# Kernel tuning notes

Hardware: AMD Instinct MI355X
Metric: run time of the kernel (lower is better)

Reference implementation:

```python
import jax, jax.numpy as jnp
import numpy as np

N_QUBITS = 9
N_CIR = 8
CHUNK = 256  # 2**(N_QUBITS-1)
DIM = 512    # 2**N_QUBITS

# Fixed gate sequence (kind, param_index, wires) transcribed from the qnode.
GATES = []
GATES += [("ry", i, (i,)) for i in range(9)]
GATES += [("rx", 9 + i, (i,)) for i in range(9)]
GATES += [("xx", 18 + k, w) for k, w in enumerate([(0,1),(8,7),(1,2),(7,6),(2,3),(6,5),(3,4),(5,4)])]
GATES += [("cry", 26 + k, w) for k, w in enumerate([(0,1),(1,2),(2,3),(8,7),(7,6),(6,5),(5,4),(3,4)])]
GATES += [("ry", 34 + i, (i,)) for i in range(9)]
GATES += [("xy", 43 + k, w) for k, w in enumerate([(4,3),(4,5),(3,2),(5,6),(2,1),(6,7),(1,0),(7,8)])]
GATES += [("crx", 51 + k, w) for k, w in enumerate([(0,1),(2,3),(5,6),(7,8),(1,2),(6,7)])]
GATES += [("rx", 57 + i, (i,)) for i in range(9)]
GATES += [("xx", 66 + k, w) for k, w in enumerate([(0,1),(8,7),(1,2),(7,6),(2,3),(6,5),(3,4),(5,4)])]
GATES += [("cry", 74 + k, w) for k, w in enumerate([(0,1),(1,2),(2,3),(8,7),(7,6),(6,5),(5,4),(3,4)])]
GATES += [("ry", 82 + i, (i,)) for i in range(9)]
GATES += [("xy", 91 + k, w) for k, w in enumerate([(4,3),(4,5),(3,2),(5,6),(2,1),(6,7),(1,0),(7,8)])]
GATES += [("crx", 99 + k, w) for k, w in enumerate([(0,1),(2,3),(5,6),(7,8),(1,2),(6,7)])]
GATES += [("rx", 105 + i, (i,)) for i in range(9)]
assert len(GATES) == 114

C64 = jnp.complex64

def _ry(t):
    c = jnp.cos(t / 2).astype(C64); s = jnp.sin(t / 2).astype(C64)
    return jnp.stack([jnp.stack([c, -s]), jnp.stack([s, c])])

def _rx(t):
    c = jnp.cos(t / 2).astype(C64); s = (-1j * jnp.sin(t / 2)).astype(C64)
    return jnp.stack([jnp.stack([c, s]), jnp.stack([s, c])])

def _xx(t):  # exp(-i t/2 XX)
    c = jnp.cos(t / 2).astype(C64); s = (-1j * jnp.sin(t / 2)).astype(C64)
    z = jnp.zeros_like(c)
    return jnp.stack([jnp.stack([c, z, z, s]), jnp.stack([z, c, s, z]),
                      jnp.stack([z, s, c, z]), jnp.stack([s, z, z, c])])

def _xy(t):  # PennyLane IsingXY
    c = jnp.cos(t / 2).astype(C64); s = (1j * jnp.sin(t / 2)).astype(C64)
    o = jnp.ones_like(c); z = jnp.zeros_like(c)
    return jnp.stack([jnp.stack([o, z, z, z]), jnp.stack([z, c, s, z]),
                      jnp.stack([z, s, c, z]), jnp.stack([z, z, z, o])])

def _ctrl(u2):  # block-diag(I2, u2): control on wires[0], target wires[1]
    z2 = jnp.zeros((2, 2), u2.dtype); i2 = jnp.eye(2, dtype=u2.dtype)
    return jnp.concatenate([jnp.concatenate([i2, z2], 1), jnp.concatenate([z2, u2], 1)], 0)

def _apply1(st, u, w):
    ax = 1 + w
    t = jnp.moveaxis(st, ax, -1)
    t = jnp.einsum('...a,ba->...b', t, u)
    return jnp.moveaxis(t, -1, ax)

def _apply2(st, u, w0, w1):
    a0, a1 = 1 + w0, 1 + w1
    t = jnp.moveaxis(st, (a0, a1), (-2, -1))
    sh = t.shape
    t = jnp.einsum('...a,ba->...b', t.reshape(sh[:-2] + (4,)), u).reshape(sh)
    return jnp.moveaxis(t, (-2, -1), (a0, a1))

def _circuit_probs(feats, qw):
    # feats: (N, 256) float32 -> analytic probs (N, 512)
    f = feats / jnp.linalg.norm(feats, axis=-1, keepdims=True)
    N = f.shape[0]
    # AmplitudeEmbedding on wires [0,1,2,3,5,6,7,8]; wire 4 stays |0>.
    st = jnp.stack([f.reshape(N, 16, 16), jnp.zeros((N, 16, 16), f.dtype)], axis=2)
    st = st.reshape((N,) + (2,) * N_QUBITS).astype(C64)
    for kind, idx, w in GATES:
        t = qw[idx]
        if kind == 'ry':
            st = _apply1(st, _ry(t), w[0])
        elif kind == 'rx':
            st = _apply1(st, _rx(t), w[0])
        elif kind == 'xx':
            st = _apply2(st, _xx(t), *w)
        elif kind == 'xy':
            st = _apply2(st, _xy(t), *w)
        elif kind == 'cry':
            st = _apply2(st, _ctrl(_ry(t)), *w)
        else:  # crx
            st = _apply2(st, _ctrl(_rx(t)), *w)
    return (st.real ** 2 + st.imag ** 2).reshape(N, DIM).astype(jnp.float32)


def setup_inputs() -> dict:
    key = jax.random.key(0)
    k1, k2 = jax.random.split(key)
    B = 4096
    return {
        "input_features": jax.random.normal(k1, (B, N_CIR * CHUNK), dtype=jnp.float32),
        "q_params": jax.random.normal(k2, (114,), dtype=jnp.float32),  # q_delta=1
    }


def reference(input_features, q_params):
    B = input_features.shape[0]
    q_in = jnp.tanh(input_features) * (np.pi / 2.0)
    chunks = q_in.reshape(B * N_CIR, CHUNK)          # per-sample split into 8 chunks of 256
    probs = _circuit_probs(chunks, q_params)          # (B*8, 512), all circuits batched
    return probs.reshape(B, 1024, 2, 2)
```

## Files before the change

### kernel.cpp

```cpp
#include <hip/hip_runtime.h>
#include <utility>

typedef __attribute__((ext_vector_type(8))) short short8;
typedef __attribute__((ext_vector_type(4))) float f32x4;
typedef unsigned short u16;

#define NROW 32768
#define KDIM 256
#define NOUT 512

static constexpr unsigned char cGK[114] = {
  0,0,0,0,0,0,0,0,0,
  1,1,1,1,1,1,1,1,1,
  2,2,2,2,2,2,2,2,
  4,4,4,4,4,4,4,4,
  0,0,0,0,0,0,0,0,0,
  3,3,3,3,3,3,3,3,
  5,5,5,5,5,5,
  1,1,1,1,1,1,1,1,1,
  2,2,2,2,2,2,2,2,
  4,4,4,4,4,4,4,4,
  0,0,0,0,0,0,0,0,0,
  3,3,3,3,3,3,3,3,
  5,5,5,5,5,5,
  1,1,1,1,1,1,1,1,1
};
static constexpr unsigned char cGW0[114] = {
  0,1,2,3,4,5,6,7,8,
  0,1,2,3,4,5,6,7,8,
  0,8,1,7,2,6,3,5,
  0,1,2,8,7,6,5,3,
  0,1,2,3,4,5,6,7,8,
  4,4,3,5,2,6,1,7,
  0,2,5,7,1,6,
  0,1,2,3,4,5,6,7,8,
  0,8,1,7,2,6,3,5,
  0,1,2,8,7,6,5,3,
  0,1,2,3,4,5,6,7,8,
  4,4,3,5,2,6,1,7,
  0,2,5,7,1,6,
  0,1,2,3,4,5,6,7,8
};
static constexpr unsigned char cGW1[114] = {
  0,0,0,0,0,0,0,0,0,
  0,0,0,0,0,0,0,0,0,
  1,7,2,6,3,5,4,4,
  1,2,3,7,6,5,4,4,
  0,0,0,0,0,0,0,0,0,
  3,5,2,6,1,7,0,8,
  1,3,6,8,2,7,
  0,0,0,0,0,0,0,0,0,
  1,7,2,6,3,5,4,4,
  1,2,3,7,6,5,4,4,
  0,0,0,0,0,0,0,0,0,
  3,5,2,6,1,7,0,8,
  1,3,6,8,2,7,
  0,0,0,0,0,0,0,0,0
};

__device__ __forceinline__ u16 f2bf(float f) {
  unsigned int u = __float_as_uint(f);
  u = (u + 0x7fffu + ((u >> 16) & 1u)) >> 16;
  return (u16)u;
}
__device__ __forceinline__ float bf2f(u16 b) {
  return __uint_as_float(((unsigned int)b) << 16);
}

__device__ __forceinline__ float fast_tanh(float x) {
  float xc = fminf(x, 15.f);
  float e = __expf(2.f * xc);
  return 1.f - 2.f * __builtin_amdgcn_rcpf(e + 1.f);
}

typedef const __attribute__((address_space(1))) unsigned int* gptr_t;
typedef __attribute__((address_space(3))) unsigned int* lptr_t;
__device__ __forceinline__ void gload16(const void* g, void* l) {
  __builtin_amdgcn_global_load_lds((gptr_t)g, (lptr_t)l, 16, 0, 0);
}

template <int G>
__device__ __forceinline__ void apply_gate(float (&re)[8], float (&im)[8],
                                           float c0v, float s0v, float c1v,
                                           float s1v, int l) {
  constexpr int kind = cGK[G];
  constexpr int p0 = 8 - cGW0[G];
  constexpr int p1 = 8 - cGW1[G];
  constexpr int m = (kind <= 1) ? (1 << p0)
                  : (kind <= 3) ? ((1 << p0) | (1 << p1))
                  : (1 << p1);
  constexpr int ml = m & 63;
  constexpr int mr = m >> 6;
  float c = __shfl((G < 64) ? c0v : c1v, G & 63, 64);
  float s = __shfl((G < 64) ? s0v : s1v, G & 63, 64);
  float br[8], bi[8];
  #pragma unroll
  for (int r = 0; r < 8; ++r) { br[r] = re[r ^ mr]; bi[r] = im[r ^ mr]; }
  if constexpr (ml != 0) {
    #pragma unroll
    for (int r = 0; r < 8; ++r) {
      br[r] = __shfl_xor(br[r], ml, 64);
      bi[r] = __shfl_xor(bi[r], ml, 64);
    }
  }
  #pragma unroll
  for (int r = 0; r < 8; ++r) {
    const int idx = (r << 6) | l;
    float nre, nim;
    if constexpr (kind == 0) {
      float sg = ((idx >> p0) & 1) ? s : -s;
      nre = c * re[r] + sg * br[r];
      nim = c * im[r] + sg * bi[r];
    } else if constexpr (kind == 1 || kind == 2) {
      nre = c * re[r] + s * bi[r];
      nim = c * im[r] - s * br[r];
    } else if constexpr (kind == 3) {
      bool ap = (((idx >> p0) ^ (idx >> p1)) & 1) != 0;
      nre = ap ? (c * re[r] - s * bi[r]) : re[r];
      nim = ap ? (c * im[r] + s * br[r]) : im[r];
    } else if constexpr (kind == 4) {
      bool ap = ((idx >> p0) & 1) != 0;
      float sg = ((idx >> p1) & 1) ? s : -s;
      nre = ap ? (c * re[r] + sg * br[r]) : re[r];
      nim = ap ? (c * im[r] + sg * bi[r]) : im[r];
    } else {
      bool ap = ((idx >> p0) & 1) != 0;
      nre = ap ? (c * re[r] + s * bi[r]) : re[r];
      nim = ap ? (c * im[r] - s * br[r]) : im[r];
    }
    re[r] = nre; im[r] = nim;
  }
}

template <int... Gs>
__device__ __forceinline__ void apply_all(std::integer_sequence<int, Gs...>,
                                          float (&re)[8], float (&im)[8],
                                          float c0v, float s0v, float c1v,
                                          float s1v, int l) {
  (apply_gate<Gs>(re, im, c0v, s0v, c1v, s1v, l), ...);
}

__global__ void __launch_bounds__(256) build_b(const float* __restrict__ qp,
                                               u16* __restrict__ BreT,
                                               u16* __restrict__ BimT) {
  int tid = threadIdx.x;
  int l = tid & 63;
  int k = blockIdx.x * 4 + (tid >> 6);
  float a0 = qp[l] * 0.5f;
  float a1 = (l < 50) ? qp[l + 64] * 0.5f : 0.f;
  float c0v = cosf(a0), s0v = sinf(a0);
  float c1v = cosf(a1), s1v = sinf(a1);

  int col = ((k >> 4) << 5) | (k & 15);
  float re[8], im[8];
  #pragma unroll
  for (int r = 0; r < 8; ++r) {
    re[r] = (r == (col >> 6) && l == (col & 63)) ? 1.f : 0.f;
    im[r] = 0.f;
  }
  apply_all(std::make_integer_sequence<int, 114>{}, re, im, c0v, s0v, c1v,
            s1v, l);
  #pragma unroll
  for (int r = 0; r < 8; ++r) {
    int j = (r << 6) | l;
    BreT[(size_t)j * KDIM + k] = f2bf(re[r]);
    BimT[(size_t)j * KDIM + k] = f2bf(im[r]);
  }
}

__global__ void __launch_bounds__(256) gemm_fused(
    const float* __restrict__ x, const u16* __restrict__ BreT,
    const u16* __restrict__ BimT, float* __restrict__ out) {
  __shared__ __align__(16) char lds[65536 + 272];
  char* sA = lds;
  float* rowsum = (float*)(lds + 65536);
  int tid = threadIdx.x;
  int l = tid & 63;
  int w = tid >> 6;
  int bid = blockIdx.x;
  int panel = (bid & 7) * 64 + (bid >> 3);
  int row0 = panel * 64;
  const float H = 1.5707963267948966f;

  #define STAGEB(bsel, it)                                                    \
    {                                                                         \
      int nb_ = (it) >> 2, t_ = (it) & 3;                                     \
      char* b_ = lds + 32768 + (bsel) * 16384;                                \
      _Pragma("unroll") for (int i = 0; i < 2; ++i) {                         \
        int sg = w * 2 + i;                                                   \
        int rn = sg * 8 + (l >> 3);                                           \
        int chunk = (l & 7) ^ (rn & 7);                                       \
        size_t off = (size_t)(nb_ * 64 + rn) * KDIM + t_ * 64 + chunk * 8;    \
        gload16(BreT + off, b_ + sg * 1024);                                  \
        gload16(BimT + off, b_ + 8192 + sg * 1024);                           \
      }                                                                       \
    }

  STAGEB(0, 0);

  #pragma unroll
  for (int p = 0; p < 8; ++p) {
    int r = p * 8 + w * 2 + (l >> 5);
    const float* xp = x + (size_t)(row0 + r) * KDIM + (l & 31) * 8;
    float4 v0 = *(const float4*)xp;
    float4 v1 = *(const float4*)(xp + 4);
    u16 b[8];
    b[0] = f2bf(fast_tanh(v0.x) * H); b[1] = f2bf(fast_tanh(v0.y) * H);
    b[2] = f2bf(fast_tanh(v0.z) * H); b[3] = f2bf(fast_tanh(v0.w) * H);
    b[4] = f2bf(fast_tanh(v1.x) * H); b[5] = f2bf(fast_tanh(v1.y) * H);
    b[6] = f2bf(fast_tanh(v1.z) * H); b[7] = f2bf(fast_tanh(v1.w) * H);
    float ss = 0.f;
    short8 pk;
    #pragma unroll
    for (int e = 0; e < 8; ++e) {
      float rr = bf2f(b[e]);
      ss += rr * rr;
      pk[e] = (short)b[e];
    }
    int cS = (l & 31) ^ (r & 7);
    *(short8*)(sA + r * 512 + cS * 16) = pk;
    #pragma unroll
    for (int o = 16; o; o >>= 1) ss += __shfl_xor(ss, o, 64);
    if ((l & 31) == 0) rowsum[r] = ss;
  }
  asm volatile("s_waitcnt vmcnt(0)" ::: "memory");
  __syncthreads();

  short8 aR[4][2];
  {
    int row = w * 16 + (l & 15);
    #pragma unroll
    for (int t = 0; t < 4; ++t)
      #pragma unroll
      for (int kk = 0; kk < 2; ++kk) {
        int c = t * 8 + kk * 4 + (l >> 4);
        int cS = c ^ (row & 7);
        aR[t][kk] = *(const short8*)(sA + row * 512 + cS * 16);
      }
  }

  for (int nb = 0; nb < 8; ++nb) {
    f32x4 accre[4] = {};
    f32x4 accim[4] = {};
    #pragma unroll
    for (int t = 0; t < 4; ++t) {
      const int it = nb * 4 + t;
      const int buf = it & 1;
      if (it < 31) STAGEB(buf ^ 1, it + 1);
      char* bre = lds + 32768 + buf * 16384;
      char* bim = bre + 8192;
      #pragma unroll
      for (int kk = 0; kk < 2; ++kk) {
        short8 brF[4], biF[4];
        #pragma unroll
        for (int nc = 0; nc < 4; ++nc) {
          int rn = nc * 16 + (l & 15);
          int chunk = (kk * 4 + (l >> 4)) ^ (rn & 7);
          brF[nc] = *(const short8*)(bre + rn * 128 + chunk * 16);
          biF[nc] = *(const short8*)(bim + rn * 128 + chunk * 16);
        }
        #pragma unroll
        for (int nc = 0; nc < 4; ++nc) {
          accre[nc] = __builtin_amdgcn_mfma_f32_16x16x32_bf16(
              aR[t][kk], brF[nc], accre[nc], 0, 0, 0);
          accim[nc] = __builtin_amdgcn_mfma_f32_16x16x32_bf16(
              aR[t][kk], biF[nc], accim[nc], 0, 0, 0);
        }
      }
      asm volatile("s_waitcnt vmcnt(0)" ::: "memory");
      __syncthreads();
    }
    #pragma unroll
    for (int reg = 0; reg < 4; ++reg) {
      int lrow = w * 16 + (l >> 4) * 4 + reg;
      float inv = 1.0f / rowsum[lrow];
      #pragma unroll
      for (int nc = 0; nc < 4; ++nc) {
        float re = accre[nc][reg];
        float im = accim[nc][reg];
        out[(size_t)(row0 + lrow) * NOUT + nb * 64 + nc * 16 + (l & 15)] =
            (re * re + im * im) * inv;
      }
    }
  }
  #undef STAGEB
}

extern "C" void kernel_launch(void* const* d_in, const int* in_sizes, int n_in,
                              void* d_out, int out_size, void* d_ws,
                              size_t ws_size, hipStream_t stream) {
  const float* x = (const float*)d_in[0];
  const float* qp = (const float*)d_in[1];
  float* out = (float*)d_out;
  char* ws = (char*)d_ws;
  u16* BreT = (u16*)ws;
  u16* BimT = (u16*)(ws + (256u << 10));

  hipLaunchKernelGGL(build_b, dim3(64), dim3(256), 0, stream, qp, BreT, BimT);
  hipLaunchKernelGGL(gemm_fused, dim3(512), dim3(256), 0, stream, x, BreT,
                     BimT, out);
}
```

Before: 61.58 us.

## Retile GEMM to 128-row panels split over two N-halves, A loaded directly to registers

Each block now covers 128 rows and half of the 512 output columns, so two blocks share a row panel. The A operand goes from global memory straight into MFMA register fragments instead of through a 64KB LDS stage. This cuts LDS use to about 17KB, which should allow more blocks per CU and removes the LDS round trip for A. Row-sum reciprocals are computed once up front, and outputs use nontemporal stores. In exchange, each row panel's tanh/bf16 conversion is done twice (once per N-half), x is read twice, and each wave holds more A registers.

```diff
diff --git a/kernel.cpp b/kernel.cpp
--- a/kernel.cpp
+++ b/kernel.cpp
@@ -171,119 +171,120 @@
 __global__ void __launch_bounds__(256) gemm_fused(
     const float* __restrict__ x, const u16* __restrict__ BreT,
     const u16* __restrict__ BimT, float* __restrict__ out) {
-  __shared__ __align__(16) char lds[65536 + 272];
-  char* sA = lds;
-  float* rowsum = (float*)(lds + 65536);
+  __shared__ __align__(16) char lds[16896];
+  float* inv = (float*)(lds + 16384);
   int tid = threadIdx.x;
   int l = tid & 63;
   int w = tid >> 6;
   int bid = blockIdx.x;
-  int panel = (bid & 7) * 64 + (bid >> 3);
-  int row0 = panel * 64;
+  int panel = ((bid >> 4) << 3) | (bid & 7);
+  int nh = (bid >> 3) & 1;
+  int row0 = panel * 128;
   const float H = 1.5707963267948966f;
 
-  #define STAGEB(bsel, it)                                                    \
+  #define STAGE(u)                                                            \
     {                                                                         \
-      int nb_ = (it) >> 2, t_ = (it) & 3;                                     \
-      char* b_ = lds + 32768 + (bsel) * 16384;                                \
-      _Pragma("unroll") for (int i = 0; i < 2; ++i) {                         \
-        int sg = w * 2 + i;                                                   \
-        int rn = sg * 8 + (l >> 3);                                           \
-        int chunk = (l & 7) ^ (rn & 7);                                       \
-        size_t off = (size_t)(nb_ * 64 + rn) * KDIM + t_ * 64 + chunk * 8;    \
-        gload16(BreT + off, b_ + sg * 1024);                                  \
-        gload16(BimT + off, b_ + 8192 + sg * 1024);                           \
-      }                                                                       \
-    }
-
-  STAGEB(0, 0);
-
-  #pragma unroll
-  for (int p = 0; p < 8; ++p) {
-    int r = p * 8 + w * 2 + (l >> 5);
-    const float* xp = x + (size_t)(row0 + r) * KDIM + (l & 31) * 8;
-    float4 v0 = *(const float4*)xp;
-    float4 v1 = *(const float4*)(xp + 4);
-    u16 b[8];
-    b[0] = f2bf(fast_tanh(v0.x) * H); b[1] = f2bf(fast_tanh(v0.y) * H);
-    b[2] = f2bf(fast_tanh(v0.z) * H); b[3] = f2bf(fast_tanh(v0.w) * H);
-    b[4] = f2bf(fast_tanh(v1.x) * H); b[5] = f2bf(fast_tanh(v1.y) * H);
-    b[6] = f2bf(fast_tanh(v1.z) * H); b[7] = f2bf(fast_tanh(v1.w) * H);
-    float ss = 0.f;
-    short8 pk;
-    #pragma unroll
-    for (int e = 0; e < 8; ++e) {
-      float rr = bf2f(b[e]);
-      ss += rr * rr;
-      pk[e] = (short)b[e];
-    }
-    int cS = (l & 31) ^ (r & 7);
-    *(short8*)(sA + r * 512 + cS * 16) = pk;
-    #pragma unroll
-    for (int o = 16; o; o >>= 1) ss += __shfl_xor(ss, o, 64);
-    if ((l & 31) == 0) rowsum[r] = ss;
+      int nb_ = (u) >> 2, t_ = (u) & 3;                                       \
+      char* d_ = lds + ((u) & 1) * 8192;                                      \
+      int rn = w * 8 + (l >> 3);                                              \
+      int ch = (l & 7) ^ (rn & 7);                                            \
+      size_t off = (size_t)(nh * 256 + nb_ * 32 + rn) * KDIM + t_ * 64 +      \
+                   ch * 8;                                                    \
+      gload16(BreT + off, d_ + w * 1024);                                     \
+      gload16(BimT + off, d_ + 4096 + w * 1024);                              \
+    }
+
+  STAGE(0);
+
+  short8 aR[2][4][2];
+  float ss[2] = {0.f, 0.f};
+  {
+    int arow = w * 32 + (l & 15);
+    int kc = (l >> 4) * 8;
+    #pragma unroll
+    for (int m = 0; m < 2; ++m)
+      #pragma unroll
+      for (int t = 0; t < 4; ++t)
+        #pragma unroll
+        for (int kk = 0; kk < 2; ++kk) {
+          const float* xp = x + (size_t)(row0 + arow + m * 16) * KDIM +
+                            t * 64 + kk * 32 + kc;
+          float4 v0 = *(const float4*)xp;
+          float4 v1 = *(const float4*)(xp + 4);
+          u16 b[8];
+          b[0] = f2bf(fast_tanh(v0.x) * H); b[1] = f2bf(fast_tanh(v0.y) * H);
+          b[2] = f2bf(fast_tanh(v0.z) * H); b[3] = f2bf(fast_tanh(v0.w) * H);
+          b[4] = f2bf(fast_tanh(v1.x) * H); b[5] = f2bf(fast_tanh(v1.y) * H);
+          b[6] = f2bf(fast_tanh(v1.z) * H); b[7] = f2bf(fast_tanh(v1.w) * H);
+          short8 pk;
+          #pragma unroll
+          for (int e = 0; e < 8; ++e) {
+            float rr = bf2f(b[e]);
+            ss[m] += rr * rr;
+            pk[e] = (short)b[e];
+          }
+          aR[m][t][kk] = pk;
+        }
+    #pragma unroll
+    for (int m = 0; m < 2; ++m) {
+      ss[m] += __shfl_xor(ss[m], 16, 64);
+      ss[m] += __shfl_xor(ss[m], 32, 64);
+      if (l < 16) inv[w * 32 + m * 16 + l] = 1.0f / ss[m];
+    }
   }
   asm volatile("s_waitcnt vmcnt(0)" ::: "memory");
   __syncthreads();
 
-  short8 aR[4][2];
-  {
-    int row = w * 16 + (l & 15);
-    #pragma unroll
-    for (int t = 0; t < 4; ++t)
+  for (int nb = 0; nb < 8; ++nb) {
+    f32x4 accre[2][2] = {};
+    f32x4 accim[2][2] = {};
+    #pragma unroll
+    for (int t = 0; t < 4; ++t) {
+      const int u = nb * 4 + t;
+      if (u < 31) STAGE(u + 1);
+      char* bre = lds + (u & 1) * 8192;
+      char* bim = bre + 4096;
       #pragma unroll
       for (int kk = 0; kk < 2; ++kk) {
-        int c = t * 8 + kk * 4 + (l >> 4);
-        int cS = c ^ (row & 7);
-        aR[t][kk] = *(const short8*)(sA + row * 512 + cS * 16);
-      }
-  }
-
-  for (int nb = 0; nb < 8; ++nb) {
-    f32x4 accre[4] = {};
-    f32x4 accim[4] = {};
-    #pragma unroll
-    for (int t = 0; t < 4; ++t) {
-      const int it = nb * 4 + t;
-      const int buf = it & 1;
-      if (it < 31) STAGEB(buf ^ 1, it + 1);
-      char* bre = lds + 32768 + buf * 16384;
-      char* bim = bre + 8192;
-      #pragma unroll
-      for (int kk = 0; kk < 2; ++kk) {
-        short8 brF[4], biF[4];
+        short8 brF[2], biF[2];
         #pragma unroll
-        for (int nc = 0; nc < 4; ++nc) {
+        for (int nc = 0; nc < 2; ++nc) {
           int rn = nc * 16 + (l & 15);
-          int chunk = (kk * 4 + (l >> 4)) ^ (rn & 7);
-          brF[nc] = *(const short8*)(bre + rn * 128 + chunk * 16);
-          biF[nc] = *(const short8*)(bim + rn * 128 + chunk * 16);
+          int ch = (kk * 4 + (l >> 4)) ^ (rn & 7);
+          brF[nc] = *(const short8*)(bre + rn * 128 + ch * 16);
+          biF[nc] = *(const short8*)(bim + rn * 128 + ch * 16);
         }
         #pragma unroll
-        for (int nc = 0; nc < 4; ++nc) {
-          accre[nc] = __builtin_amdgcn_mfma_f32_16x16x32_bf16(
-              aR[t][kk], brF[nc], accre[nc], 0, 0, 0);
-          accim[nc] = __builtin_amdgcn_mfma_f32_16x16x32_bf16(
-              aR[t][kk], biF[nc], accim[nc], 0, 0, 0);
-        }
+        for (int m = 0; m < 2; ++m)
+          #pragma unroll
+          for (int nc = 0; nc < 2; ++nc) {
+            accre[m][nc] = __builtin_amdgcn_mfma_f32_16x16x32_bf16(
+                aR[m][t][kk], brF[nc], accre[m][nc], 0, 0, 0);
+            accim[m][nc] = __builtin_amdgcn_mfma_f32_16x16x32_bf16(
+                aR[m][t][kk], biF[nc], accim[m][nc], 0, 0, 0);
+          }
       }
       asm volatile("s_waitcnt vmcnt(0)" ::: "memory");
       __syncthreads();
     }
     #pragma unroll
-    for (int reg = 0; reg < 4; ++reg) {
-      int lrow = w * 16 + (l >> 4) * 4 + reg;
-      float inv = 1.0f / rowsum[lrow];
+    for (int m = 0; m < 2; ++m)
       #pragma unroll
-      for (int nc = 0; nc < 4; ++nc) {
-        float re = accre[nc][reg];
-        float im = accim[nc][reg];
-        out[(size_t)(row0 + lrow) * NOUT + nb * 64 + nc * 16 + (l & 15)] =
-            (re * re + im * im) * inv;
+      for (int reg = 0; reg < 4; ++reg) {
+        int r = w * 32 + m * 16 + (l >> 4) * 4 + reg;
+        float iv = inv[r];
+        #pragma unroll
+        for (int nc = 0; nc < 2; ++nc) {
+          float re = accre[m][nc][reg];
+          float im = accim[m][nc][reg];
+          __builtin_nontemporal_store(
+              (re * re + im * im) * iv,
+              out + (size_t)(row0 + r) * NOUT + nh * 256 + nb * 32 + nc * 16 +
+                  (l & 15));
+        }
       }
-    }
-  }
-  #undef STAGEB
+  }
+  #undef STAGE
 }
 
 extern "C" void kernel_launch(void* const* d_in, const int* in_sizes, int n_in,
```

After: 58.50 us. 5.0% less time.
